# Kernel optimization log

Hardware: AMD Instinct MI355X
Metric: run time of the kernel (lower is better)

Reference implementation:

```python
import jax, jax.numpy as jnp
import numpy as np

N_ROUTING = 3


def squash(x):
    # Faithful to source: tf.norm with axis=None -> global norm over the whole tensor
    n = jnp.linalg.norm(x)
    return n / (1.0 + n * n) * x


def setup_inputs() -> dict:
    key = jax.random.key(0)
    k1, k2 = jax.random.split(key)
    B, n_input, dim_input = 128, 1152, 32
    n_output, dim_output = 32, 32
    x = jax.random.normal(k1, (B, n_input, dim_input), dtype=jnp.float32)
    # glorot_uniform-like init for W: (n_input, n_output, dim_output, dim_input)
    limit = np.sqrt(6.0 / (dim_input + dim_output)).astype(np.float32)
    W = jax.random.uniform(k2, (n_input, n_output, dim_output, dim_input),
                           dtype=jnp.float32, minval=-limit, maxval=limit)
    return {"x": x, "W": W}


def reference(x, W):
    B, n_input, _ = x.shape
    n_output = W.shape[1]
    # x_hat[b,i,o,d] = sum_k W[i,o,d,k] * x[b,i,k]   (replaces map_fn/batch_dot)
    x_hat = jnp.einsum('iodk,bik->biod', W, x)
    x_hat_sg = jax.lax.stop_gradient(x_hat)
    b = jnp.zeros((B, n_input, n_output), dtype=x.dtype)
    v = None
    for it in range(N_ROUTING):
        c = jax.nn.softmax(b, axis=2)                      # over output capsules
        xh = x_hat if it == N_ROUTING - 1 else x_hat_sg    # grads only on last iter
        s = jnp.einsum('bio,biod->bod', c, xh)
        v = squash(s)
        if it < N_ROUTING - 1:
            b = b + jnp.einsum('biod,bod->bio', x_hat_sg, v)
    return v
```

## Files before the change

### kernel.cpp

```cpp
#include <hip/hip_runtime.h>
#include <math.h>

#define NI 1152
#define NO 32
#define DI 32
#define DO 32
#define NBATCH 128

constexpr int IBLK = 36;
constexpr int NIB  = 32;
constexpr int BBLK = 16;
constexpr int NBB  = NBATCH / BBLK;
constexpr int LDS_FLOATS = 32 * 1024 + 16 * 32;

typedef __attribute__((ext_vector_type(8))) short short8v;
typedef __attribute__((ext_vector_type(4))) float f32x4;
typedef __attribute__((ext_vector_type(2))) float f32x2;

__device__ __forceinline__ void gll16(const float* g, float* l) {
  __builtin_amdgcn_global_load_lds(
      (const __attribute__((address_space(1))) void*)(const void*)g,
      (__attribute__((address_space(3))) void*)(void*)l, 16, 0, 0);
}

#define WAITV(n) do { asm volatile("s_waitcnt vmcnt(" #n ")" ::: "memory"); \
  __builtin_amdgcn_sched_barrier(0); } while (0)
#define LGKM0() do { asm volatile("s_waitcnt lgkmcnt(0)" ::: "memory"); \
  __builtin_amdgcn_sched_barrier(0); } while (0)
#define BARLDS() do { asm volatile("s_waitcnt lgkmcnt(0)" ::: "memory"); \
  __builtin_amdgcn_sched_barrier(0); __builtin_amdgcn_s_barrier(); } while (0)

struct S3 { short hi, mi, lo; };
__device__ __forceinline__ S3 split3(float w) {
  S3 r;
  const unsigned u = __float_as_uint(w);
  r.hi = (short)(u >> 16);
  const float r1 = w - __uint_as_float(u & 0xFFFF0000u);
  const unsigned r1u = __float_as_uint(r1);
  r.mi = (short)(r1u >> 16);
  const float r2 = r1 - __uint_as_float(r1u & 0xFFFF0000u);
  r.lo = (short)(__float_as_uint(r2) >> 16);
  return r;
}

__device__ __forceinline__ void stage_w_half(const float* __restrict__ Wg,
                                             float* __restrict__ Wt,
                                             int i, int h, int w, size_t wsrc_lane) {
  const float* sb = Wg + (size_t)i * 32768 + wsrc_lane + (size_t)h * 2048;
  float* db = Wt + (size_t)(w * 1024 + h * 512) * 4;
#pragma unroll
  for (int r = 0; r < 8; ++r)
    gll16(sb + r * 256, db + r * 256);
}

template<int IT>
__global__ __launch_bounds__(512, 2)
void caps_pass(const float* __restrict__ xg, const float* __restrict__ Wg,
               float* __restrict__ spart, const float* __restrict__ s_in,
               const float* __restrict__ fsc, float* __restrict__ bbuf)
{
  extern __shared__ float lds[];
  float* Wt = lds;
  float* bl = lds + 32 * 1024;

  const int t = threadIdx.x, w = t >> 6, l = t & 63;
  const int ib = blockIdx.x, bb = blockIdx.y, b0 = bb * BBLK;

  const size_t wsrc_lane = (size_t)(w * 128 + (l >> 3)) * 32
                         + (size_t)(((l & 7) ^ (l >> 3)) * 4);

  int colf[4];
#pragma unroll
  for (int s = 0; s < 4; ++s)
    colf[s] = ((((l >> 4) * 2 + (s >> 1)) ^ (l & 7)) * 4) + (s & 1) * 2;

  const float* xbase = xg + (size_t)(b0 + (l & 15)) * (NI * DI) + (l >> 4) * 8;

  f32x4 vfrag[8];
  if constexpr (IT > 0) {
    const float f = fsc[0];
    const float* vp = s_in + (size_t)bb * 16384 + w * 2048 + l * 4;
#pragma unroll
    for (int tl = 0; tl < 8; ++tl) {
      f32x4 sv = *(const f32x4*)(vp + tl * 256);
      vfrag[tl] = sv * f;
    }
  }
  WAITV(0);

  f32x4 sreg[8];
#pragma unroll
  for (int tl = 0; tl < 8; ++tl) sreg[tl] = (f32x4){0.f, 0.f, 0.f, 0.f};

  const int i0 = ib * IBLK;
  stage_w_half(Wg, Wt, i0, 0, w, wsrc_lane);
  f32x4 xa = *(const f32x4*)(xbase + (size_t)i0 * DI);
  f32x4 xb = *(const f32x4*)(xbase + (size_t)i0 * DI + 4);
  stage_w_half(Wg, Wt, i0, 1, w, wsrc_lane);

  for (int ii = 0; ii < IBLK; ++ii) {
    const int i = i0 + ii;
    const int inext = i0 + ((ii + 1 < IBLK) ? ii + 1 : ii);

    f32x4 acc[8];
#pragma unroll
    for (int tl = 0; tl < 8; ++tl) acc[tl] = (f32x4){0.f, 0.f, 0.f, 0.f};

    short8v xhi, xmi, xlo;
    f32x4 xna, xnb;

#pragma unroll
    for (int h = 0; h < 2; ++h) {
      f32x2 wf[4][4];
      if (h == 0) {
        WAITV(8);
#pragma unroll
        for (int e = 0; e < 4; ++e) {
          S3 sa = split3(xa[e]);
          xhi[e] = sa.hi; xmi[e] = sa.mi; xlo[e] = sa.lo;
          S3 sb2 = split3(xb[e]);
          xhi[4 + e] = sb2.hi; xmi[4 + e] = sb2.mi; xlo[4 + e] = sb2.lo;
        }
      } else {
        WAITV(10);
      }
#pragma unroll
      for (int tl = 0; tl < 4; ++tl) {
        const float* rp = Wt + (size_t)(w * 128 + (h * 4 + tl) * 16 + (l & 15)) * 32;
#pragma unroll
        for (int s = 0; s < 4; ++s) wf[tl][s] = *(const f32x2*)(rp + colf[s]);
      }
      LGKM0();

      if (h == 0) {
        stage_w_half(Wg, Wt, inext, 0, w, wsrc_lane);
        xna = *(const f32x4*)(xbase + (size_t)inext * DI);
        xnb = *(const f32x4*)(xbase + (size_t)inext * DI + 4);
      } else {
        stage_w_half(Wg, Wt, inext, 1, w, wsrc_lane);
      }

#pragma unroll
      for (int tl = 0; tl < 4; ++tl) {
        const int tloc = h * 4 + tl;
        short8v whi, wmi, wlo;
#pragma unroll
        for (int s = 0; s < 4; ++s) {
          S3 s0 = split3(wf[tl][s].x);
          whi[2 * s] = s0.hi; wmi[2 * s] = s0.mi; wlo[2 * s] = s0.lo;
          S3 s1 = split3(wf[tl][s].y);
          whi[2 * s + 1] = s1.hi; wmi[2 * s + 1] = s1.mi; wlo[2 * s + 1] = s1.lo;
        }
        f32x4 a = acc[tloc];
        a = __builtin_amdgcn_mfma_f32_16x16x32_bf16(whi, xhi, a, 0, 0, 0);
        a = __builtin_amdgcn_mfma_f32_16x16x32_bf16(whi, xmi, a, 0, 0, 0);
        a = __builtin_amdgcn_mfma_f32_16x16x32_bf16(wmi, xhi, a, 0, 0, 0);
        a = __builtin_amdgcn_mfma_f32_16x16x32_bf16(whi, xlo, a, 0, 0, 0);
        a = __builtin_amdgcn_mfma_f32_16x16x32_bf16(wlo, xhi, a, 0, 0, 0);
        a = __builtin_amdgcn_mfma_f32_16x16x32_bf16(wmi, xmi, a, 0, 0, 0);
        acc[tloc] = a;
      }
    }
    xa = xna; xb = xnb;

    if constexpr (IT == 0) {
#pragma unroll
      for (int tl = 0; tl < 8; ++tl) sreg[tl] += acc[tl] * 0.03125f;
    } else {
      float bup[4];
#pragma unroll
      for (int j = 0; j < 4; ++j) {
        f32x4 p = acc[2 * j] * vfrag[2 * j] + acc[2 * j + 1] * vfrag[2 * j + 1];
        float v = p[0] + p[1] + p[2] + p[3];
        v += __shfl_xor(v, 16);
        v += __shfl_xor(v, 32);
        bup[j] = v;
      }
      if (l < 16) {
#pragma unroll
        for (int j = 0; j < 4; ++j) bl[l * 32 + w * 4 + j] = bup[j];
      }
      BARLDS();

      {
        const int bo = t >> 5, oo = t & 31;
        float lg = bl[bo * 32 + oo];
        if constexpr (IT == 2)
          lg += bbuf[(size_t)(b0 + bo) * (NI * NO) + (size_t)i * NO + oo];
        if constexpr (IT == 1)
          bbuf[(size_t)(b0 + bo) * (NI * NO) + (size_t)i * NO + oo] = lg;
        float mx = lg;
#pragma unroll
        for (int m = 1; m < 32; m <<= 1) mx = fmaxf(mx, __shfl_xor(mx, m));
        const float e = __expf(lg - mx);
        float sm = e;
#pragma unroll
        for (int m = 1; m < 32; m <<= 1) sm += __shfl_xor(sm, m);
        bl[bo * 32 + oo] = e / sm;
      }
      BARLDS();

#pragma unroll
      for (int j = 0; j < 4; ++j) {
        const float cj = bl[(l & 15) * 32 + w * 4 + j];
        sreg[2 * j]     += acc[2 * j]     * cj;
        sreg[2 * j + 1] += acc[2 * j + 1] * cj;
      }
    }
  }

  WAITV(0);

  {
    float* op = spart + ((size_t)ib * NBB + bb) * 16384 + w * 2048 + l * 4;
#pragma unroll
    for (int tl = 0; tl < 8; ++tl) *(f32x4*)(op + tl * 256) = sreg[tl];
  }
}

__global__ __launch_bounds__(256)
void caps_red(const float* __restrict__ spart, float* __restrict__ s,
              float* __restrict__ part)
{
  const int t = threadIdx.x;
  const size_t e = (size_t)blockIdx.x * 256 + t;
  float a = 0.f;
#pragma unroll
  for (int ibk = 0; ibk < NIB; ++ibk) a += spart[(size_t)ibk * (NBATCH * 1024) + e];
  s[e] = a;
  float qv = a * a;
#pragma unroll
  for (int m = 1; m < 64; m <<= 1) qv += __shfl_xor(qv, m);
  __shared__ float red[4];
  if ((t & 63) == 0) red[t >> 6] = qv;
  __syncthreads();
  if (t == 0) part[blockIdx.x] = red[0] + red[1] + red[2] + red[3];
}

__global__ __launch_bounds__(256)
void caps_norm(const float* __restrict__ part, float* __restrict__ fsc)
{
  const int t = threadIdx.x;
  float qv = part[t] + part[t + 256];
#pragma unroll
  for (int m = 1; m < 64; m <<= 1) qv += __shfl_xor(qv, m);
  __shared__ float red[4];
  if ((t & 63) == 0) red[t >> 6] = qv;
  __syncthreads();
  if (t == 0) {
    const float S = red[0] + red[1] + red[2] + red[3];
    fsc[0] = sqrtf(S) / (1.f + S);
  }
}

__global__ __launch_bounds__(256)
void caps_out(const float* __restrict__ s, const float* __restrict__ fsc,
              float* __restrict__ out)
{
  const int E = blockIdx.x * 256 + threadIdx.x;
  const float v = s[E] * fsc[0];
  const int r = E & 3, ll = (E >> 2) & 63, tl = (E >> 8) & 7,
            w = (E >> 11) & 7, bb = E >> 14;
  const int b = bb * 16 + (ll & 15);
  const int od = w * 128 + tl * 16 + (ll >> 4) * 4 + r;
  out[b * 1024 + od] = v;
}

extern "C" void kernel_launch(void* const* d_in, const int* in_sizes, int n_in,
                              void* d_out, int out_size, void* d_ws, size_t ws_size,
                              hipStream_t stream)
{
  const float* xg = (const float*)d_in[0];
  const float* Wg = (const float*)d_in[1];
  float* out = (float*)d_out;

  float* wsf   = (float*)d_ws;
  float* spart = wsf;
  float* s     = spart + (size_t)NIB * NBATCH * 1024;
  float* part  = s + (size_t)NBATCH * 1024;
  float* fsc   = part + 512;
  float* bbuf  = fsc + 1;

  const int ldsB = LDS_FLOATS * 4;
  (void)hipFuncSetAttribute(reinterpret_cast<const void*>(&caps_pass<0>),
                            hipFuncAttributeMaxDynamicSharedMemorySize, ldsB);
  (void)hipFuncSetAttribute(reinterpret_cast<const void*>(&caps_pass<1>),
                            hipFuncAttributeMaxDynamicSharedMemorySize, ldsB);
  (void)hipFuncSetAttribute(reinterpret_cast<const void*>(&caps_pass<2>),
                            hipFuncAttributeMaxDynamicSharedMemorySize, ldsB);

  dim3 pg(NIB, NBB);

  caps_pass<0><<<pg, 512, ldsB, stream>>>(xg, Wg, spart, s, fsc, bbuf);
  caps_red <<<512, 256, 0, stream>>>(spart, s, part);
  caps_norm<<<1,   256, 0, stream>>>(part, fsc);

  caps_pass<1><<<pg, 512, ldsB, stream>>>(xg, Wg, spart, s, fsc, bbuf);
  caps_red <<<512, 256, 0, stream>>>(spart, s, part);
  caps_norm<<<1,   256, 0, stream>>>(part, fsc);

  caps_pass<2><<<pg, 512, ldsB, stream>>>(xg, Wg, spart, s, fsc, bbuf);
  caps_red <<<512, 256, 0, stream>>>(spart, s, part);
  caps_norm<<<1,   256, 0, stream>>>(part, fsc);

  caps_out <<<512, 256, 0, stream>>>(s, fsc, out);
}
```

Before: 389.6 us.

## Pre-split W into bf16 hi/mid/lo planes once and read them directly in passes

Adds a pre-pass that splits W into three bf16 planes laid out in MFMA fragment order, written to the workspace. The three routing passes then load these fragments straight from global memory, with no LDS staging and no per-pass split of W. The intent is to do the split once instead of once per routing pass and to drop the LDS traffic. The cost is an extra kernel that writes and later rereads 1.5x W's bytes (three bf16 planes) on every call, and the faster path runs only when the workspace is large enough.

```diff
diff --git a/kernel.cpp b/kernel.cpp
--- a/kernel.cpp
+++ b/kernel.cpp
@@ -11,22 +11,11 @@
 constexpr int NIB  = 32;
 constexpr int BBLK = 16;
 constexpr int NBB  = NBATCH / BBLK;
-constexpr int LDS_FLOATS = 32 * 1024 + 16 * 32;
 
 typedef __attribute__((ext_vector_type(8))) short short8v;
 typedef __attribute__((ext_vector_type(4))) float f32x4;
 typedef __attribute__((ext_vector_type(2))) float f32x2;
 
-__device__ __forceinline__ void gll16(const float* g, float* l) {
-  __builtin_amdgcn_global_load_lds(
-      (const __attribute__((address_space(1))) void*)(const void*)g,
-      (__attribute__((address_space(3))) void*)(void*)l, 16, 0, 0);
-}
-
-#define WAITV(n) do { asm volatile("s_waitcnt vmcnt(" #n ")" ::: "memory"); \
-  __builtin_amdgcn_sched_barrier(0); } while (0)
-#define LGKM0() do { asm volatile("s_waitcnt lgkmcnt(0)" ::: "memory"); \
-  __builtin_amdgcn_sched_barrier(0); } while (0)
 #define BARLDS() do { asm volatile("s_waitcnt lgkmcnt(0)" ::: "memory"); \
   __builtin_amdgcn_sched_barrier(0); __builtin_amdgcn_s_barrier(); } while (0)
 
@@ -43,6 +32,159 @@
   return r;
 }
 
+
+__global__ __launch_bounds__(256)
+void caps_pack3(const float* __restrict__ Wg, short8v* __restrict__ P0,
+                short8v* __restrict__ P1, short8v* __restrict__ P2)
+{
+  const size_t j8 = (size_t)blockIdx.x * 256 + threadIdx.x;
+  const float* src = Wg + j8 * 8;
+  const f32x4 a = *(const f32x4*)src;
+  const f32x4 b = *(const f32x4*)(src + 4);
+  short8v hi, mi, lo;
+#pragma unroll
+  for (int e = 0; e < 4; ++e) {
+    S3 r0 = split3(a[e]); hi[e] = r0.hi;     mi[e] = r0.mi;     lo[e] = r0.lo;
+    S3 r1 = split3(b[e]); hi[4 + e] = r1.hi; mi[4 + e] = r1.mi; lo[4 + e] = r1.lo;
+  }
+  P0[j8] = hi;
+  P1[j8] = mi;
+  P2[j8] = lo;
+}
+
+template<int IT>
+__global__ __launch_bounds__(512, 2)
+void caps_passd(const float* __restrict__ xg, const short8v* __restrict__ P0,
+                const short8v* __restrict__ P1, const short8v* __restrict__ P2,
+                float* __restrict__ spart, const float* __restrict__ s_in,
+                const float* __restrict__ fsc, float* __restrict__ bbuf)
+{
+  __shared__ float bl[16 * 32];
+
+  const int t = threadIdx.x, w = t >> 6, l = t & 63;
+  const int ib = blockIdx.x, bb = blockIdx.y, b0 = bb * BBLK;
+
+  const float* xbase = xg + (size_t)(b0 + (l & 15)) * (NI * DI) + (l >> 4) * 8;
+
+  const size_t wbase = (size_t)(w * 128 + (l & 15)) * 4 + (l >> 4);
+
+  f32x4 vfrag[8];
+  if constexpr (IT > 0) {
+    const float f = fsc[0];
+    const float* vp = s_in + (size_t)bb * 16384 + w * 2048 + l * 4;
+#pragma unroll
+    for (int tl = 0; tl < 8; ++tl) {
+      f32x4 sv = *(const f32x4*)(vp + tl * 256);
+      vfrag[tl] = sv * f;
+    }
+  }
+
+  f32x4 sreg[8];
+#pragma unroll
+  for (int tl = 0; tl < 8; ++tl) sreg[tl] = (f32x4){0.f, 0.f, 0.f, 0.f};
+
+  const int i0 = ib * IBLK;
+
+  for (int ii = 0; ii < IBLK; ++ii) {
+    const int i = i0 + ii;
+
+    const f32x4 xa = *(const f32x4*)(xbase + (size_t)i * DI);
+    const f32x4 xb = *(const f32x4*)(xbase + (size_t)i * DI + 4);
+    short8v xhi, xmi, xlo;
+#pragma unroll
+    for (int e = 0; e < 4; ++e) {
+      S3 r0 = split3(xa[e]);
+      xhi[e] = r0.hi; xmi[e] = r0.mi; xlo[e] = r0.lo;
+      S3 r1 = split3(xb[e]);
+      xhi[4 + e] = r1.hi; xmi[4 + e] = r1.mi; xlo[4 + e] = r1.lo;
+    }
+
+    f32x4 acc[8];
+#pragma unroll
+    for (int tl = 0; tl < 8; ++tl) acc[tl] = (f32x4){0.f, 0.f, 0.f, 0.f};
+
+    const size_t pb = (size_t)i * 4096 + wbase;
+#pragma unroll
+    for (int tl = 0; tl < 8; ++tl) {
+      const size_t widx = pb + (size_t)tl * 64;
+      const short8v wh = P0[widx];
+      const short8v wm = P1[widx];
+      const short8v wo = P2[widx];
+      f32x4 a = acc[tl];
+      a = __builtin_amdgcn_mfma_f32_16x16x32_bf16(wh, xhi, a, 0, 0, 0);
+      a = __builtin_amdgcn_mfma_f32_16x16x32_bf16(wh, xmi, a, 0, 0, 0);
+      a = __builtin_amdgcn_mfma_f32_16x16x32_bf16(wm, xhi, a, 0, 0, 0);
+      a = __builtin_amdgcn_mfma_f32_16x16x32_bf16(wh, xlo, a, 0, 0, 0);
+      a = __builtin_amdgcn_mfma_f32_16x16x32_bf16(wo, xhi, a, 0, 0, 0);
+      a = __builtin_amdgcn_mfma_f32_16x16x32_bf16(wm, xmi, a, 0, 0, 0);
+      acc[tl] = a;
+    }
+
+    if constexpr (IT == 0) {
+#pragma unroll
+      for (int tl = 0; tl < 8; ++tl) sreg[tl] += acc[tl] * 0.03125f;
+    } else {
+      float bup[4];
+#pragma unroll
+      for (int j = 0; j < 4; ++j) {
+        f32x4 p = acc[2 * j] * vfrag[2 * j] + acc[2 * j + 1] * vfrag[2 * j + 1];
+        float v = p[0] + p[1] + p[2] + p[3];
+        v += __shfl_xor(v, 16);
+        v += __shfl_xor(v, 32);
+        bup[j] = v;
+      }
+      if (l < 16) {
+#pragma unroll
+        for (int j = 0; j < 4; ++j) bl[l * 32 + w * 4 + j] = bup[j];
+      }
+      BARLDS();
+      {
+        const int bo = t >> 5, oo = t & 31;
+        float lg = bl[bo * 32 + oo];
+        if constexpr (IT == 2)
+          lg += bbuf[(size_t)(b0 + bo) * (NI * NO) + (size_t)i * NO + oo];
+        if constexpr (IT == 1)
+          bbuf[(size_t)(b0 + bo) * (NI * NO) + (size_t)i * NO + oo] = lg;
+        float mx = lg;
+#pragma unroll
+        for (int m = 1; m < 32; m <<= 1) mx = fmaxf(mx, __shfl_xor(mx, m));
+        const float e = __expf(lg - mx);
+        float sm = e;
+#pragma unroll
+        for (int m = 1; m < 32; m <<= 1) sm += __shfl_xor(sm, m);
+        bl[bo * 32 + oo] = e / sm;
+      }
+      BARLDS();
+#pragma unroll
+      for (int j = 0; j < 4; ++j) {
+        const float cj = bl[(l & 15) * 32 + w * 4 + j];
+        sreg[2 * j]     += acc[2 * j]     * cj;
+        sreg[2 * j + 1] += acc[2 * j + 1] * cj;
+      }
+    }
+  }
+
+  {
+    float* op = spart + ((size_t)ib * NBB + bb) * 16384 + w * 2048 + l * 4;
+#pragma unroll
+    for (int tl = 0; tl < 8; ++tl) *(f32x4*)(op + tl * 256) = sreg[tl];
+  }
+}
+
+
+constexpr int LDS_FLOATS_S = 32 * 1024 + 16 * 32;
+
+__device__ __forceinline__ void gll16(const float* g, float* l) {
+  __builtin_amdgcn_global_load_lds(
+      (const __attribute__((address_space(1))) void*)(const void*)g,
+      (__attribute__((address_space(3))) void*)(void*)l, 16, 0, 0);
+}
+
+#define WAITV(n) do { asm volatile("s_waitcnt vmcnt(" #n ")" ::: "memory"); \
+  __builtin_amdgcn_sched_barrier(0); } while (0)
+#define LGKM0() do { asm volatile("s_waitcnt lgkmcnt(0)" ::: "memory"); \
+  __builtin_amdgcn_sched_barrier(0); } while (0)
+
 __device__ __forceinline__ void stage_w_half(const float* __restrict__ Wg,
                                              float* __restrict__ Wt,
                                              int i, int h, int w, size_t wsrc_lane) {
@@ -55,9 +197,9 @@
 
 template<int IT>
 __global__ __launch_bounds__(512, 2)
-void caps_pass(const float* __restrict__ xg, const float* __restrict__ Wg,
-               float* __restrict__ spart, const float* __restrict__ s_in,
-               const float* __restrict__ fsc, float* __restrict__ bbuf)
+void caps_pass_s(const float* __restrict__ xg, const float* __restrict__ Wg,
+                 float* __restrict__ spart, const float* __restrict__ s_in,
+                 const float* __restrict__ fsc, float* __restrict__ bbuf)
 {
   extern __shared__ float lds[];
   float* Wt = lds;
@@ -68,7 +210,6 @@
 
   const size_t wsrc_lane = (size_t)(w * 128 + (l >> 3)) * 32
                          + (size_t)(((l & 7) ^ (l >> 3)) * 4);
-
   int colf[4];
 #pragma unroll
   for (int s = 0; s < 4; ++s)
@@ -181,7 +322,6 @@
         for (int j = 0; j < 4; ++j) bl[l * 32 + w * 4 + j] = bup[j];
       }
       BARLDS();
-
       {
         const int bo = t >> 5, oo = t & 31;
         float lg = bl[bo * 32 + oo];
@@ -199,7 +339,6 @@
         bl[bo * 32 + oo] = e / sm;
       }
       BARLDS();
-
 #pragma unroll
       for (int j = 0; j < 4; ++j) {
         const float cj = bl[(l & 15) * 32 + w * 4 + j];
@@ -210,13 +349,13 @@
   }
 
   WAITV(0);
-
   {
     float* op = spart + ((size_t)ib * NBB + bb) * 16384 + w * 2048 + l * 4;
 #pragma unroll
     for (int tl = 0; tl < 8; ++tl) *(f32x4*)(op + tl * 256) = sreg[tl];
   }
 }
+
 
 __global__ __launch_bounds__(256)
 void caps_red(const float* __restrict__ spart, float* __restrict__ s,
@@ -266,6 +405,7 @@
   out[b * 1024 + od] = v;
 }
 
+
 extern "C" void kernel_launch(void* const* d_in, const int* in_sizes, int n_in,
                               void* d_out, int out_size, void* d_ws, size_t ws_size,
                               hipStream_t stream)
@@ -274,34 +414,66 @@
   const float* Wg = (const float*)d_in[1];
   float* out = (float*)d_out;
 
-  float* wsf   = (float*)d_ws;
-  float* spart = wsf;
-  float* s     = spart + (size_t)NIB * NBATCH * 1024;
-  float* part  = s + (size_t)NBATCH * 1024;
-  float* fsc   = part + 512;
-  float* bbuf  = fsc + 1;
-
-  const int ldsB = LDS_FLOATS * 4;
-  (void)hipFuncSetAttribute(reinterpret_cast<const void*>(&caps_pass<0>),
-                            hipFuncAttributeMaxDynamicSharedMemorySize, ldsB);
-  (void)hipFuncSetAttribute(reinterpret_cast<const void*>(&caps_pass<1>),
-                            hipFuncAttributeMaxDynamicSharedMemorySize, ldsB);
-  (void)hipFuncSetAttribute(reinterpret_cast<const void*>(&caps_pass<2>),
-                            hipFuncAttributeMaxDynamicSharedMemorySize, ldsB);
-
-  dim3 pg(NIB, NBB);
-
-  caps_pass<0><<<pg, 512, ldsB, stream>>>(xg, Wg, spart, s, fsc, bbuf);
-  caps_red <<<512, 256, 0, stream>>>(spart, s, part);
-  caps_norm<<<1,   256, 0, stream>>>(part, fsc);
-
-  caps_pass<1><<<pg, 512, ldsB, stream>>>(xg, Wg, spart, s, fsc, bbuf);
-  caps_red <<<512, 256, 0, stream>>>(spart, s, part);
-  caps_norm<<<1,   256, 0, stream>>>(part, fsc);
-
-  caps_pass<2><<<pg, 512, ldsB, stream>>>(xg, Wg, spart, s, fsc, bbuf);
-  caps_red <<<512, 256, 0, stream>>>(spart, s, part);
-  caps_norm<<<1,   256, 0, stream>>>(part, fsc);
-
-  caps_out <<<512, 256, 0, stream>>>(s, fsc, out);
-}
+  const size_t planeE  = 4718592;
+  const size_t bbufFl  = (size_t)NBATCH * NI * NO;
+  const size_t need_fast = planeE * 3 * 16 +
+      ((size_t)NIB * NBB * 16384 + 131072 + 512 + 4 + bbufFl) * 4;
+
+  if (ws_size >= need_fast) {
+    short8v* P0 = (short8v*)d_ws;
+    short8v* P1 = P0 + planeE;
+    short8v* P2 = P1 + planeE;
+    float* spart = (float*)(P2 + planeE);
+    float* S    = spart + (size_t)NIB * NBB * 16384;
+    float* part = S + 131072;
+    float* fsc  = part + 512;
+    float* bbuf = fsc + 4;
+
+    dim3 pg(NIB, NBB);
+    caps_pack3<<<18432, 256, 0, stream>>>(Wg, P0, P1, P2);
+
+    caps_passd<0><<<pg, 512, 0, stream>>>(xg, P0, P1, P2, spart, S, fsc, bbuf);
+    caps_red <<<512, 256, 0, stream>>>(spart, S, part);
+    caps_norm<<<1,   256, 0, stream>>>(part, fsc);
+
+    caps_passd<1><<<pg, 512, 0, stream>>>(xg, P0, P1, P2, spart, S, fsc, bbuf);
+    caps_red <<<512, 256, 0, stream>>>(spart, S, part);
+    caps_norm<<<1,   256, 0, stream>>>(part, fsc);
+
+    caps_passd<2><<<pg, 512, 0, stream>>>(xg, P0, P1, P2, spart, S, fsc, bbuf);
+    caps_red <<<512, 256, 0, stream>>>(spart, S, part);
+    caps_norm<<<1,   256, 0, stream>>>(part, fsc);
+
+    caps_out <<<512, 256, 0, stream>>>(S, fsc, out);
+  } else {
+    float* wsf   = (float*)d_ws;
+    float* spart = wsf;
+    float* S     = spart + (size_t)NIB * NBATCH * 1024;
+    float* part  = S + (size_t)NBATCH * 1024;
+    float* fsc   = part + 512;
+    float* bbuf  = fsc + 1;
+
+    const int ldsB = LDS_FLOATS_S * 4;
+    (void)hipFuncSetAttribute(reinterpret_cast<const void*>(&caps_pass_s<0>),
+                              hipFuncAttributeMaxDynamicSharedMemorySize, ldsB);
+    (void)hipFuncSetAttribute(reinterpret_cast<const void*>(&caps_pass_s<1>),
+                              hipFuncAttributeMaxDynamicSharedMemorySize, ldsB);
+    (void)hipFuncSetAttribute(reinterpret_cast<const void*>(&caps_pass_s<2>),
+                              hipFuncAttributeMaxDynamicSharedMemorySize, ldsB);
+
+    dim3 pg(NIB, NBB);
+    caps_pass_s<0><<<pg, 512, ldsB, stream>>>(xg, Wg, spart, S, fsc, bbuf);
+    caps_red <<<512, 256, 0, stream>>>(spart, S, part);
+    caps_norm<<<1,   256, 0, stream>>>(part, fsc);
+
+    caps_pass_s<1><<<pg, 512, ldsB, stream>>>(xg, Wg, spart, S, fsc, bbuf);
+    caps_red <<<512, 256, 0, stream>>>(spart, S, part);
+    caps_norm<<<1,   256, 0, stream>>>(part, fsc);
+
+    caps_pass_s<2><<<pg, 512, ldsB, stream>>>(xg, Wg, spart, S, fsc, bbuf);
+    caps_red <<<512, 256, 0, stream>>>(spart, S, part);
+    caps_norm<<<1,   256, 0, stream>>>(part, fsc);
+
+    caps_out <<<512, 256, 0, stream>>>(S, fsc, out);
+  }
+}
```

After: 778.3 us. 99.8% more time.
